# Kernel optimization log

Hardware: AMD Instinct MI355X
Metric: run time of the kernel (lower is better)

Reference implementation:

```python
import jax, jax.numpy as jnp
import numpy as np

IN_FEATS, N_HIDDEN, NUM_LAYERS, N_CLASSES, CLS_HIDDEN = 166, 76, 2, 2, 510
T, N, E = 3, 100000, 1600000
RRELU_SLOPE = (1.0 / 8.0 + 1.0 / 3.0) / 2.0  # eval-mode RReLU = leaky relu with mean slope


def setup_inputs() -> dict:
    key = jax.random.key(0)
    ks = jax.random.split(key, 24)
    d = {}
    d['feats'] = jax.random.normal(ks[0], (T, N, IN_FEATS), jnp.float32)
    d['src'] = jax.random.randint(ks[1], (T, E), 0, N, jnp.int32)
    d['dst'] = jax.random.randint(ks[2], (T, E), 0, N, jnp.int32)
    # TopK scorers (uniform +-1/sqrt(feats))
    s0 = 1.0 / np.sqrt(IN_FEATS)
    s1 = 1.0 / np.sqrt(N_HIDDEN)
    d['scorer0'] = jax.random.uniform(ks[3], (IN_FEATS, 1), jnp.float32, -s0, s0)
    d['scorer1'] = jax.random.uniform(ks[4], (N_HIDDEN, 1), jnp.float32, -s1, s1)
    # GCN weights (xavier-ish)
    d['gcn_w0'] = jax.random.normal(ks[5], (IN_FEATS, N_HIDDEN), jnp.float32) * np.sqrt(2.0 / (IN_FEATS + N_HIDDEN))
    d['gcn_w1'] = jax.random.normal(ks[6], (N_HIDDEN, N_HIDDEN), jnp.float32) * np.sqrt(2.0 / (2 * N_HIDDEN))
    # GRU params, torch layout: W_ih [3H, H_in], W_hh [3H, H], gate order (r, z, n)
    g = 1.0 / np.sqrt(N_HIDDEN)
    H3 = 3 * N_HIDDEN
    d['gru0_wih'] = jax.random.uniform(ks[7], (H3, N_HIDDEN), jnp.float32, -g, g)
    d['gru0_whh'] = jax.random.uniform(ks[8], (H3, N_HIDDEN), jnp.float32, -g, g)
    d['gru0_bih'] = jax.random.uniform(ks[9], (H3,), jnp.float32, -g, g)
    d['gru0_bhh'] = jax.random.uniform(ks[10], (H3,), jnp.float32, -g, g)
    d['gru1_wih'] = jax.random.uniform(ks[11], (H3, N_HIDDEN), jnp.float32, -g, g)
    d['gru1_whh'] = jax.random.uniform(ks[12], (H3, N_HIDDEN), jnp.float32, -g, g)
    d['gru1_bih'] = jax.random.uniform(ks[13], (H3,), jnp.float32, -g, g)
    d['gru1_bhh'] = jax.random.uniform(ks[14], (H3,), jnp.float32, -g, g)
    # MLP
    m1 = 1.0 / np.sqrt(N_HIDDEN)
    m2 = 1.0 / np.sqrt(CLS_HIDDEN)
    d['mlp_w1'] = jax.random.uniform(ks[15], (N_HIDDEN, CLS_HIDDEN), jnp.float32, -m1, m1)
    d['mlp_b1'] = jax.random.uniform(ks[16], (CLS_HIDDEN,), jnp.float32, -m1, m1)
    d['mlp_w2'] = jax.random.uniform(ks[17], (CLS_HIDDEN, N_CLASSES), jnp.float32, -m2, m2)
    d['mlp_b2'] = jax.random.uniform(ks[18], (N_CLASSES,), jnp.float32, -m2, m2)
    return d


def _topk_pool(x, scorer, k):
    # x: [N, F]; returns X_tilde: [F, k]
    scores = (x @ scorer).ravel() / jnp.linalg.norm(scorer)
    vals, idx = jax.lax.top_k(scores, k)
    out = x[idx] * jnp.tanh(vals)[:, None]  # [k, F]
    return out.T


def _gru_step(x, h, wih, whh, bih, bhh):
    # x: [B, H_in], h: [B, H]; torch GRU gate order r, z, n
    gx = x @ wih.T + bih
    gh = h @ whh.T + bhh
    H = h.shape[1]
    rx, zx, nx = gx[:, :H], gx[:, H:2 * H], gx[:, 2 * H:]
    rh, zh, nh = gh[:, :H], gh[:, H:2 * H], gh[:, 2 * H:]
    r = jax.nn.sigmoid(rx + rh)
    z = jax.nn.sigmoid(zx + zh)
    n = jnp.tanh(nx + r * nh)
    return (1.0 - z) * n + z * h


def _graph_conv(x, W, src, dst, n_nodes):
    # DGL GraphConv, norm='both', bias=False, RReLU (eval) activation
    deg_out = jnp.zeros((n_nodes,), x.dtype).at[src].add(1.0)
    deg_in = jnp.zeros((n_nodes,), x.dtype).at[dst].add(1.0)
    norm_src = jnp.clip(deg_out, 1.0, None) ** -0.5
    norm_dst = jnp.clip(deg_in, 1.0, None) ** -0.5
    h = (x * norm_src[:, None]) @ W  # project first (small out dim)
    agg = jax.ops.segment_sum(h[src], dst, num_segments=n_nodes)
    out = agg * norm_dst[:, None]
    return jnp.where(out >= 0, out, out * RRELU_SLOPE)


def reference(feats, src, dst, scorer0, scorer1, gcn_w0, gcn_w1,
              gru0_wih, gru0_whh, gru0_bih, gru0_bhh,
              gru1_wih, gru1_whh, gru1_bih, gru1_bhh,
              mlp_w1, mlp_b1, mlp_w2, mlp_b2):
    scorers = [scorer0, scorer1]
    gcn_ws = [gcn_w0, gcn_w1]
    grus = [(gru0_wih, gru0_whh, gru0_bih, gru0_bhh),
            (gru1_wih, gru1_whh, gru1_bih, gru1_bhh)]
    feat_list = [feats[t] for t in range(T)]
    for i in range(NUM_LAYERS):
        W = gcn_ws[i]
        wih, whh, bih, bhh = grus[i]
        for t in range(T):
            x_tilde = _topk_pool(feat_list[t], scorers[i], N_HIDDEN)  # [F, k]
            W = _gru_step(x_tilde, W, wih, whh, bih, bhh)  # evolve weights
            feat_list[t] = _graph_conv(feat_list[t], W, src[t], dst[t], N)
    h = feat_list[-1]
    h = jax.nn.relu(h @ mlp_w1 + mlp_b1)
    return h @ mlp_w2 + mlp_b2
```

## Files before the change

kernel.cpp:

```cpp
#include <hip/hip_runtime.h>
#include <math.h>

#define NN 100000
#define EE 1600000
#define F0 166
#define HID 76
#define H3 228
#define CHID 510
#define SLOPE 0.22916666666666666f
#define CAND_MAX 4096
#define NBIN 4096
#define HPAD 20
#define MJ 256

#define BSH 9
#define BSZ 512
#define NBKT 196
#define CH 4096
#define NCHK 391

__device__ __forceinline__ unsigned f2key(float f){
    unsigned u = __float_as_uint(f);
    return (u & 0x80000000u) ? ~u : (u | 0x80000000u);
}
__device__ __forceinline__ float key2f(unsigned k){
    unsigned u = (k & 0x80000000u) ? (k & 0x7fffffffu) : ~k;
    return __uint_as_float(u);
}

__global__ void scorer_norms_k(const float* __restrict__ s0, const float* __restrict__ s1,
                               float* __restrict__ outn){
    __shared__ float red[256];
    int tid = threadIdx.x;
    float a = 0.f;
    for (int k = tid; k < F0; k += 256) a += s0[k]*s0[k];
    red[tid] = a; __syncthreads();
    for (int s = 128; s > 0; s >>= 1){ if (tid < s) red[tid] += red[tid+s]; __syncthreads(); }
    if (tid == 0) outn[0] = 1.0f/sqrtf(red[0]);
    __syncthreads();
    float b = 0.f;
    for (int k = tid; k < HID; k += 256) b += s1[k]*s1[k];
    red[tid] = b; __syncthreads();
    for (int s = 128; s > 0; s >>= 1){ if (tid < s) red[tid] += red[tid+s]; __syncthreads(); }
    if (tid == 0) outn[1] = 1.0f/sqrtf(red[0]);
}

__global__ void pad_k(const float* __restrict__ w1, const float* __restrict__ b1,
                      const float* __restrict__ w2, float* __restrict__ w1t,
                      float* __restrict__ b1p, float* __restrict__ w2p){
    int idx = blockIdx.x*256 + threadIdx.x;
    if (idx < 512*HID){
        int j = idx / HID, k = idx - j*HID;
        w1t[idx] = (j < CHID) ? w1[k*CHID + j] : 0.f;
    }
    if (idx < 512)  b1p[idx] = (idx < CHID)   ? b1[idx] : 0.f;
    if (idx < 1024) w2p[idx] = (idx < CHID*2) ? w2[idx] : 0.f;
}


__global__ __launch_bounds__(256) void p1_hist_k(const int* __restrict__ src, const int* __restrict__ dst,
                                                 int* __restrict__ bhS, int* __restrict__ bhD){
    __shared__ int hS[NBKT], hD[NBKT];
    int t = blockIdx.y, blk = blockIdx.x, tid = threadIdx.x;
    for (int i = tid; i < NBKT; i += 256){ hS[i] = 0; hD[i] = 0; }
    __syncthreads();
    size_t ebase = (size_t)t*EE + (size_t)blk*CH;
    int m = EE - blk*CH; if (m > CH) m = CH;
    for (int j = tid; j < m; j += 256){
        atomicAdd(&hS[src[ebase + j] >> BSH], 1);
        atomicAdd(&hD[dst[ebase + j] >> BSH], 1);
    }
    __syncthreads();
    for (int i = tid; i < NBKT; i += 256){
        bhS[((size_t)t*NBKT + i)*NCHK + blk] = hS[i];
        bhD[((size_t)t*NBKT + i)*NCHK + blk] = hD[i];
    }
}

__global__ __launch_bounds__(512) void p2_scan_k(int* __restrict__ bhS, int* __restrict__ bhD,
                                                 int* __restrict__ ctS, int* __restrict__ ctD){
    __shared__ int sd[512];
    int b = blockIdx.x, t = blockIdx.y, tid = threadIdx.x;
    for (int a = 0; a < 2; a++){
        int* bh = a ? bhD : bhS;
        int* ct = a ? ctD : ctS;
        int* row = bh + ((size_t)t*NBKT + b)*NCHK;
        int v = (tid < NCHK) ? row[tid] : 0;
        sd[tid] = v; __syncthreads();
        for (int off = 1; off < 512; off <<= 1){
            int x = (tid >= off) ? sd[tid - off] : 0;
            __syncthreads();
            sd[tid] += x;
            __syncthreads();
        }
        if (tid < NCHK) row[tid] = sd[tid] - v;
        if (tid == 511) ct[t*NBKT + b] = sd[511];
        __syncthreads();
    }
}

__global__ __launch_bounds__(256) void p3_base_k(const int* __restrict__ ctS, const int* __restrict__ ctD,
                                                 int* __restrict__ bbS, int* __restrict__ bbD){
    __shared__ int sd[256];
    int tid = threadIdx.x;
    for (int a = 0; a < 2; a++){
        const int* ct = a ? ctD : ctS;
        int* bb = a ? bbD : bbS;
        for (int t = 0; t < 3; t++){
            int v = (tid < NBKT) ? ct[t*NBKT + tid] : 0;
            sd[tid] = v; __syncthreads();
            for (int off = 1; off < 256; off <<= 1){
                int x = (tid >= off) ? sd[tid - off] : 0;
                __syncthreads();
                sd[tid] += x;
                __syncthreads();
            }
            if (tid < NBKT) bb[t*(NBKT+1) + tid] = sd[tid] - v;
            if (tid == 0)   bb[t*(NBKT+1) + NBKT] = EE;
            __syncthreads();
        }
    }
}

__global__ __launch_bounds__(256) void p4_scatter_k(const int* __restrict__ src, const int* __restrict__ dst,
                                                    const int* __restrict__ bhS, const int* __restrict__ bhD,
                                                    const int* __restrict__ bbS, const int* __restrict__ bbD,
                                                    int* __restrict__ srcpart,
                                                    unsigned long long* __restrict__ pairpart){
    __shared__ int baseS[NBKT], baseD[NBKT], cS[NBKT], cD[NBKT];
    int t = blockIdx.y, blk = blockIdx.x, tid = threadIdx.x;
    for (int i = tid; i < NBKT; i += 256){
        baseS[i] = bbS[t*(NBKT+1) + i] + bhS[((size_t)t*NBKT + i)*NCHK + blk];
        baseD[i] = bbD[t*(NBKT+1) + i] + bhD[((size_t)t*NBKT + i)*NCHK + blk];
        cS[i] = 0; cD[i] = 0;
    }
    __syncthreads();
    size_t ebase = (size_t)t*EE + (size_t)blk*CH;
    int m = EE - blk*CH; if (m > CH) m = CH;
    int* sp = srcpart + (size_t)t*EE;
    unsigned long long* pp = pairpart + (size_t)t*EE;
    for (int j = tid; j < m; j += 256){
        int s = src[ebase + j], d = dst[ebase + j];
        int bs = s >> BSH, bd = d >> BSH;
        int r0 = atomicAdd(&cS[bs], 1);
        sp[baseS[bs] + r0] = s;
        int r1 = atomicAdd(&cD[bd], 1);
        pp[baseD[bd] + r1] = ((unsigned long long)(unsigned)s << 32) | (unsigned)d;
    }
}

__global__ __launch_bounds__(256) void p5_degO_k(const int* __restrict__ srcpart,
                                                 const int* __restrict__ bbS,
                                                 float* __restrict__ nO){
    __shared__ int cnt[BSZ];
    int b = blockIdx.x, t = blockIdx.y, tid = threadIdx.x;
    for (int i = tid; i < BSZ; i += 256) cnt[i] = 0;
    __syncthreads();
    int st = bbS[t*(NBKT+1) + b], en = bbS[t*(NBKT+1) + b + 1];
    const int* sp = srcpart + (size_t)t*EE;
    for (int j = st + tid; j < en; j += 256) atomicAdd(&cnt[sp[j] & (BSZ-1)], 1);
    __syncthreads();
    int nb = b << BSH;
    for (int i = tid; i < BSZ; i += 256){
        int n = nb + i;
        if (n < NN){
            int o = cnt[i]; if (o < 1) o = 1;
            nO[t*NN + n] = 1.0f/sqrtf((float)o);
        }
    }
}

__global__ __launch_bounds__(512) void p6_csr_k(const unsigned long long* __restrict__ pairpart,
                                                const int* __restrict__ bbD,
                                                int* __restrict__ degI, int* __restrict__ rs,
                                                float* __restrict__ nI,
                                                int* __restrict__ col){
    __shared__ int cnt[BSZ];
    __shared__ int sc[BSZ];
    __shared__ int fc[BSZ];
    int b = blockIdx.x, t = blockIdx.y, tid = threadIdx.x;
    cnt[tid] = 0; fc[tid] = 0;
    __syncthreads();
    int st = bbD[t*(NBKT+1) + b], en = bbD[t*(NBKT+1) + b + 1];
    const unsigned long long* pp = pairpart + (size_t)t*EE;
    for (int j = st + tid; j < en; j += 512)
        atomicAdd(&cnt[(int)(pp[j] & (unsigned long long)(BSZ-1))], 1);
    __syncthreads();
    int v = cnt[tid];
    sc[tid] = v; __syncthreads();
    for (int off = 1; off < 512; off <<= 1){
        int x = (tid >= off) ? sc[tid - off] : 0;
        __syncthreads();
        sc[tid] += x;
        __syncthreads();
    }
    int ex = sc[tid] - v;
    int nb = b << BSH;
    int n = nb + tid;
    if (n < NN){
        degI[t*NN + n] = v;
        rs[t*NN + n] = st + ex;
        int ii = v; if (ii < 1) ii = 1;
        nI[t*NN + n] = 1.0f/sqrtf((float)ii);
    }
    sc[tid] = ex;
    __syncthreads();
    int* ct = col + (size_t)t*EE;
    for (int j = st + tid; j < en; j += 512){
        unsigned long long p = pp[j];
        int d = (int)(p & 0xffffffffull);
        int li = d & (BSZ-1);
        int r = atomicAdd(&fc[li], 1);
        ct[st + sc[li] + r] = (int)(p >> 32);
    }
}


template<int F, int PAD>
__global__ __launch_bounds__(256) void score_k(const float* __restrict__ x,
                                               const float* __restrict__ scorer,
                                               const float* __restrict__ invn,
                                               float* __restrict__ scores,
                                               unsigned* hist){
    __shared__ float xs[64*PAD];
    __shared__ float part[256];
    int tid = threadIdx.x;
    int n0 = blockIdx.x*64;
    int nodes = NN - n0; if (nodes > 64) nodes = 64;
    for (int idx = tid; idx < nodes*F; idx += 256){
        int n = idx / F, k = idx - n*F;
        xs[n*PAD + k] = x[(size_t)(n0+n)*F + k];
    }
    __syncthreads();
    int w = __builtin_amdgcn_readfirstlane(tid >> 6);
    int lane = tid & 63;
    int k0 = (F*w) >> 2, k1 = (F*(w+1)) >> 2;
    const float* xrow = xs + lane*PAD;
    float s = 0.f;
    for (int k = k0; k < k1; k++) s += xrow[k]*scorer[k];
    part[w*64 + lane] = s;
    __syncthreads();
    if (tid < 64 && n0 + tid < NN){
        float tot = (part[tid] + part[64+tid] + part[128+tid] + part[192+tid]) * invn[0];
        scores[n0 + tid] = tot;
        atomicAdd(&hist[f2key(tot) >> 20], 1u);
    }
}

__global__ __launch_bounds__(256) void compact_k(const float* __restrict__ scores,
                                                 const unsigned* __restrict__ hist,
                                                 float* __restrict__ cv, int* __restrict__ ci, int* cnt){
    __shared__ unsigned cs[256];
    __shared__ int thr_s;
    int tid = threadIdx.x;
    unsigned s = 0;
    int base = NBIN - 1 - tid*16;
    for (int j = 0; j < 16; j++) s += hist[base - j];
    cs[tid] = s; __syncthreads();
    if (tid == 0){
        unsigned acc = 0; int c = 0;
        for (; c < 256; c++){ if (acc + cs[c] >= 76u) break; acc += cs[c]; }
        int b = NBIN - 1 - c*16;
        int sel = 0;
        for (int j = 0; j < 16; j++){
            acc += hist[b - j];
            if (acc >= 76u){ sel = b - j; break; }
        }
        thr_s = sel;
    }
    __syncthreads();
    int thr = thr_s;
    int n = blockIdx.x*256 + tid;
    if (n >= NN) return;
    float sv = scores[n];
    if ((int)(f2key(sv) >> 20) >= thr){
        int p = atomicAdd(cnt, 1);
        if (p < CAND_MAX){ cv[p] = sv; ci[p] = n; }
    }
}

__global__ __launch_bounds__(256) void topk_k(const float* __restrict__ cv,
                                              const int* __restrict__ ci,
                                              const int* __restrict__ cnt,
                                              int* __restrict__ topidx,
                                              float* __restrict__ tanhv){
    __shared__ unsigned long long keys[CAND_MAX];
    int tid = threadIdx.x;
    int M = *cnt; if (M > CAND_MAX) M = CAND_MAX;
    for (int i = tid; i < M; i += 256)
        keys[i] = ((unsigned long long)f2key(cv[i]) << 32) | (unsigned)(~ci[i]);
    __syncthreads();
    for (int i = tid; i < M; i += 256){
        unsigned long long ki = keys[i];
        int r = 0;
        for (int j = 0; j < M; j++) r += (keys[j] > ki) ? 1 : 0;
        if (r < 76){
            topidx[r] = (int)(~(unsigned)(ki & 0xffffffffu));
            tanhv[r]  = tanhf(key2f((unsigned)(ki >> 32)));
        }
    }
}

template<int F>
__global__ void gru_k(const float* __restrict__ cur, const int* __restrict__ topidx,
                      const float* __restrict__ tanhv, float* __restrict__ W,
                      float* __restrict__ Wt,
                      const float* __restrict__ wih, const float* __restrict__ whh,
                      const float* __restrict__ bih, const float* __restrict__ bhh){
    __shared__ float xr[HID], hr[HID], gx[H3], gh[H3];
    int r = blockIdx.x, tid = threadIdx.x;
    if (tid < HID){
        xr[tid] = cur[(size_t)topidx[tid]*F + r] * tanhv[tid];
        hr[tid] = W[r*HID + tid];
    }
    __syncthreads();
    if (tid < H3){
        const float* wi = wih + tid*HID;
        const float* wh = whh + tid*HID;
        float sa = 0.f, sb = 0.f;
        for (int k = 0; k < HID; k++){ sa += xr[k]*wi[k]; sb += hr[k]*wh[k]; }
        gx[tid] = bih[tid] + sa;
        gh[tid] = bhh[tid] + sb;
    }
    __syncthreads();
    if (tid < HID){
        float rr = 1.f/(1.f + expf(-(gx[tid] + gh[tid])));
        float zz = 1.f/(1.f + expf(-(gx[HID+tid] + gh[HID+tid])));
        float nn = tanhf(gx[2*HID+tid] + rr*gh[2*HID+tid]);
        float nv = (1.f - zz)*nn + zz*hr[tid];
        W[r*HID + tid] = nv;
        int c = tid >> 2, i = tid & 3;
        Wt[(c*F + r)*4 + i] = nv;
    }
}

template<int F, int PAD, int NB>
__global__ __launch_bounds__(256) void gemm_k(const float* __restrict__ x,
                                              const float* __restrict__ Wt,
                                              const float* __restrict__ nO,
                                              float* __restrict__ h){
    __shared__ __align__(16) float xs[NB*PAD];
    int tid = threadIdx.x;
    int n0 = blockIdx.x*NB;
    int nodes = NN - n0; if (nodes > NB) nodes = NB;
    for (int idx = tid; idx < nodes*F; idx += 256){
        int n = idx / F, k = idx - n*F;
        xs[n*PAD + k] = x[(size_t)(n0+n)*F + k];
    }
    __syncthreads();
    int w = __builtin_amdgcn_readfirstlane(tid >> 6);
    int lane = tid & 63;
    int c0 = w*5;
    const float4* Wt4 = (const float4*)Wt;
    float4 accA[5], accB[5];
    #pragma unroll
    for (int c = 0; c < 5; c++){
        accA[c] = make_float4(0.f,0.f,0.f,0.f);
        accB[c] = make_float4(0.f,0.f,0.f,0.f);
    }
    const float* xA = xs + lane*PAD;
    const float* xB = xs + ((NB==128) ? (lane+64)*PAD : lane*PAD);
    for (int k = 0; k < F; k++){
        float xa = xA[k];
        float xb = 0.f;
        if constexpr (NB == 128) xb = xB[k];
        #pragma unroll
        for (int c = 0; c < 5; c++){
            float4 wv = Wt4[(c0 + c)*F + k];
            accA[c].x += xa*wv.x; accA[c].y += xa*wv.y;
            accA[c].z += xa*wv.z; accA[c].w += xa*wv.w;
            if constexpr (NB == 128){
                accB[c].x += xb*wv.x; accB[c].y += xb*wv.y;
                accB[c].z += xb*wv.z; accB[c].w += xb*wv.w;
            }
        }
    }
    int nc = (w == 3) ? 4 : 5;
    int nA = n0 + lane;
    if (nA < NN){
        float nm = nO[nA];
        float4* h4 = (float4*)h + (size_t)nA*HPAD + c0;
        for (int c = 0; c < nc; c++){
            float4 a = accA[c];
            h4[c] = make_float4(a.x*nm, a.y*nm, a.z*nm, a.w*nm);
        }
    }
    if constexpr (NB == 128){
        int nB = n0 + 64 + lane;
        if (nB < NN){
            float nm = nO[nB];
            float4* h4 = (float4*)h + (size_t)nB*HPAD + c0;
            for (int c = 0; c < nc; c++){
                float4 a = accB[c];
                h4[c] = make_float4(a.x*nm, a.y*nm, a.z*nm, a.w*nm);
            }
        }
    }
}

__global__ void agg_k(const int* __restrict__ rs, const int* __restrict__ degI,
                      const int* __restrict__ col, const float* __restrict__ h,
                      const float* __restrict__ nI, float* __restrict__ ft){
    int idx = blockIdx.x*256 + threadIdx.x;
    if (idx >= NN*19) return;
    int n = idx/19, c = idx - n*19;
    int st = rs[n], cnt = degI[n];
    const float4* h4 = (const float4*)h;
    float ax=0.f, ay=0.f, az=0.f, aw=0.f;
    int e = 0;
    for (; e + 4 <= cnt; e += 4){
        int s0 = col[st + e];
        int s1 = col[st + e + 1];
        int s2 = col[st + e + 2];
        int s3 = col[st + e + 3];
        float4 v0 = h4[(size_t)s0*HPAD + c];
        float4 v1 = h4[(size_t)s1*HPAD + c];
        float4 v2 = h4[(size_t)s2*HPAD + c];
        float4 v3 = h4[(size_t)s3*HPAD + c];
        ax += (v0.x + v1.x) + (v2.x + v3.x);
        ay += (v0.y + v1.y) + (v2.y + v3.y);
        az += (v0.z + v1.z) + (v2.z + v3.z);
        aw += (v0.w + v1.w) + (v2.w + v3.w);
    }
    for (; e < cnt; e++){
        int s = col[st + e];
        float4 v = h4[(size_t)s*HPAD + c];
        ax += v.x; ay += v.y; az += v.z; aw += v.w;
    }
    float nm = nI[n];
    ax*=nm; ay*=nm; az*=nm; aw*=nm;
    ax = ax >= 0.f ? ax : ax*SLOPE;
    ay = ay >= 0.f ? ay : ay*SLOPE;
    az = az >= 0.f ? az : az*SLOPE;
    aw = aw >= 0.f ? aw : aw*SLOPE;
    ((float4*)ft)[(size_t)n*19 + c] = make_float4(ax,ay,az,aw);
}

__global__ __launch_bounds__(1024) void mlp2_k(const float* __restrict__ ft,
                                               const float* __restrict__ w1t,
                                               const float* __restrict__ b1p,
                                               const float* __restrict__ w2p,
                                               const float* __restrict__ b2,
                                               float* __restrict__ out){
    __shared__ __align__(16) float ws[MJ*HID];
    __shared__ float w2s[MJ*2];
    __shared__ float b1s[MJ];
    int tid = threadIdx.x;
    int jbase = blockIdx.y * MJ;
    const float4* wg = (const float4*)(w1t + (size_t)jbase*HID);
    float4* wsv = (float4*)ws;
    for (int i = tid; i < MJ*HID/4; i += 1024) wsv[i] = wg[i];
    if (tid < MJ*2) w2s[tid] = w2p[jbase*2 + tid];
    if (tid < MJ)   b1s[tid] = b1p[jbase + tid];
    __syncthreads();
    int node = blockIdx.x*1024 + tid;
    if (node >= NN) return;
    float4 r[19];
    const float4* rp = (const float4*)(ft + (size_t)node*HID);
    #pragma unroll
    for (int k = 0; k < 19; k++) r[k] = rp[k];
    float acc0 = 0.f, acc1 = 0.f;
    if (jbase == 0){ acc0 = b2[0]; acc1 = b2[1]; }
    const float4* ws4 = (const float4*)ws;
    for (int g = 0; g < MJ/4; g++){
        int j0 = g*4;
        float s0 = b1s[j0], s1 = b1s[j0+1], s2 = b1s[j0+2], s3 = b1s[j0+3];
        const float4* wr = ws4 + j0*19;
        #pragma unroll
        for (int k4 = 0; k4 < 19; k4++){
            float4 rv = r[k4];
            float4 w0 = wr[k4];
            float4 w1 = wr[19 + k4];
            float4 w2v = wr[38 + k4];
            float4 w3 = wr[57 + k4];
            s0 += rv.x*w0.x + rv.y*w0.y + rv.z*w0.z + rv.w*w0.w;
            s1 += rv.x*w1.x + rv.y*w1.y + rv.z*w1.z + rv.w*w1.w;
            s2 += rv.x*w2v.x + rv.y*w2v.y + rv.z*w2v.z + rv.w*w2v.w;
            s3 += rv.x*w3.x + rv.y*w3.y + rv.z*w3.z + rv.w*w3.w;
        }
        s0 = fmaxf(s0, 0.f); s1 = fmaxf(s1, 0.f);
        s2 = fmaxf(s2, 0.f); s3 = fmaxf(s3, 0.f);
        acc0 += s0*w2s[j0*2]   + s1*w2s[j0*2+2] + s2*w2s[j0*2+4] + s3*w2s[j0*2+6];
        acc1 += s0*w2s[j0*2+1] + s1*w2s[j0*2+3] + s2*w2s[j0*2+5] + s3*w2s[j0*2+7];
    }
    atomicAdd(&out[(size_t)node*2],     acc0);
    atomicAdd(&out[(size_t)node*2 + 1], acc1);
}

extern "C" void kernel_launch(void* const* d_in, const int* in_sizes, int n_in,
                              void* d_out, int out_size, void* d_ws, size_t ws_size,
                              hipStream_t stream)
{
    (void)in_sizes; (void)n_in; (void)out_size; (void)ws_size;
    const float* feats   = (const float*)d_in[0];
    const int*   src     = (const int*)d_in[1];
    const int*   dst     = (const int*)d_in[2];
    const float* scorer0 = (const float*)d_in[3];
    const float* scorer1 = (const float*)d_in[4];
    const float* gcnw[2] = {(const float*)d_in[5],  (const float*)d_in[6]};
    const float* wih[2]  = {(const float*)d_in[7],  (const float*)d_in[11]};
    const float* whh[2]  = {(const float*)d_in[8],  (const float*)d_in[12]};
    const float* bih[2]  = {(const float*)d_in[9],  (const float*)d_in[13]};
    const float* bhh[2]  = {(const float*)d_in[10], (const float*)d_in[14]};
    const float* w1 = (const float*)d_in[15];
    const float* b1 = (const float*)d_in[16];
    const float* w2 = (const float*)d_in[17];
    const float* b2 = (const float*)d_in[18];
    float* out = (float*)d_out;

    char* p = (char*)d_ws;
    auto alloc = [&](size_t bytes) -> void* {
        void* r = (void*)p;
        p += (bytes + 255) & ~(size_t)255;
        return r;
    };
    float* ft[3];
    for (int t = 0; t < 3; t++) ft[t] = (float*)alloc((size_t)NN*HID*4);
    float* hbuf    = (float*)alloc((size_t)NN*HPAD*16);
    int*   col_all = (int*)alloc((size_t)3*EE*4);
    float* nO_all  = (float*)alloc((size_t)3*NN*4);
    float* nI_all  = (float*)alloc((size_t)3*NN*4);
    int*   rs_all  = (int*)alloc((size_t)3*NN*4);
    int*   dI_all  = (int*)alloc((size_t)3*NN*4);
    int* srcpart = (int*)alloc((size_t)3*EE*4);
    unsigned long long* pairpart = (unsigned long long*)alloc((size_t)3*EE*8);
    int* bhS = (int*)alloc((size_t)3*NBKT*NCHK*4);
    int* bhD = (int*)alloc((size_t)3*NBKT*NCHK*4);
    int* ctS = (int*)alloc((size_t)3*NBKT*4);
    int* ctD = (int*)alloc((size_t)3*NBKT*4);
    int* bbS = (int*)alloc((size_t)3*(NBKT+1)*4);
    int* bbD = (int*)alloc((size_t)3*(NBKT+1)*4);

    float*    scores = (float*)alloc((size_t)NN*4);
    float*    cv     = (float*)alloc(CAND_MAX*4);
    int*      ci     = (int*)alloc(CAND_MAX*4);
    int*      topidx = (int*)alloc(128*4);
    float*    tanhv  = (float*)alloc(128*4);
    float*    Wbuf   = (float*)alloc((size_t)F0*HID*4 + 256);
    float*    Wt     = (float*)alloc((size_t)19*F0*16 + 4096);
    float*    invn   = (float*)alloc(256);
    float*    w1t    = (float*)alloc((size_t)512*HID*4);
    float*    b1p    = (float*)alloc(512*4);
    float*    w2p    = (float*)alloc(1024*4);

    char* zbase = p;
    unsigned* hist6 = (unsigned*)alloc((size_t)6*NBIN*4);
    int*      ccnt6 = (int*)alloc(6*256);
    size_t zsize = (size_t)(p - zbase);

    const int gN  = (NN + 255)/256;
    const int gA  = (NN*19 + 255)/256;
    const int gB  = (NN + 63)/64;
    const int gB2 = (NN + 127)/128;
    const int gM  = (NN + 1023)/1024;
    const int gP  = (512*HID + 255)/256;

    hipMemsetAsync(zbase, 0, zsize, stream);
    hipMemsetAsync(out, 0, (size_t)NN*2*4, stream);
    scorer_norms_k<<<1,256,0,stream>>>(scorer0, scorer1, invn);
    pad_k<<<gP,256,0,stream>>>(w1, b1, w2, w1t, b1p, w2p);

    p1_hist_k<<<dim3(NCHK,3),256,0,stream>>>(src, dst, bhS, bhD);
    p2_scan_k<<<dim3(NBKT,3),512,0,stream>>>(bhS, bhD, ctS, ctD);
    p3_base_k<<<1,256,0,stream>>>(ctS, ctD, bbS, bbD);
    p4_scatter_k<<<dim3(NCHK,3),256,0,stream>>>(src, dst, bhS, bhD, bbS, bbD, srcpart, pairpart);
    p5_degO_k<<<dim3(NBKT,3),256,0,stream>>>(srcpart, bbS, nO_all);
    p6_csr_k<<<dim3(NBKT,3),512,0,stream>>>(pairpart, bbD, dI_all, rs_all, nI_all, col_all);

    for (int i = 0; i < 2; i++){
        hipMemcpyAsync(Wbuf, gcnw[i], (size_t)((i==0)?F0:HID)*HID*4, hipMemcpyDeviceToDevice, stream);
        for (int t = 0; t < 3; t++){
            int q = i*3 + t;
            unsigned* hist = hist6 + (size_t)q*NBIN;
            int* ccnt = ccnt6 + q*64;
            const float* cur = (i == 0) ? (feats + (size_t)t*NN*F0) : ft[t];
            if (i == 0) score_k<F0,167><<<gB,256,0,stream>>>(cur, scorer0, invn+0, scores, hist);
            else        score_k<HID,77><<<gB,256,0,stream>>>(cur, scorer1, invn+1, scores, hist);
            compact_k<<<gN,256,0,stream>>>(scores, hist, cv, ci, ccnt);
            topk_k<<<1,256,0,stream>>>(cv, ci, ccnt, topidx, tanhv);
            if (i == 0){
                gru_k<F0><<<F0,256,0,stream>>>(cur, topidx, tanhv, Wbuf, Wt, wih[i], whh[i], bih[i], bhh[i]);
                gemm_k<F0,167,64><<<gB,256,0,stream>>>(cur, Wt, nO_all + (size_t)t*NN, hbuf);
            } else {
                gru_k<HID><<<HID,256,0,stream>>>(cur, topidx, tanhv, Wbuf, Wt, wih[i], whh[i], bih[i], bhh[i]);
                gemm_k<HID,77,128><<<gB2,256,0,stream>>>(cur, Wt, nO_all + (size_t)t*NN, hbuf);
            }
            agg_k<<<gA,256,0,stream>>>(rs_all + (size_t)t*NN, dI_all + (size_t)t*NN,
                                       col_all + (size_t)t*EE, hbuf, nI_all + (size_t)t*NN, ft[t]);
        }
    }

    mlp2_k<<<dim3(gM,2),1024,0,stream>>>(ft[2], w1t, b1p, w2p, b2, out);
}
```

Baseline: 2.587 ms.

## Register-tile the classifier MLP and band-sort CSR columns by source id

New measurement: 2.517 ms. 2.7% less time.

```diff
diff --git a/kernel.cpp b/kernel.cpp
--- a/kernel.cpp
+++ b/kernel.cpp
@@ -11,13 +11,13 @@
 #define CAND_MAX 4096
 #define NBIN 4096
 #define HPAD 20
-#define MJ 256
 
 #define BSH 9
 #define BSZ 512
 #define NBKT 196
 #define CH 4096
 #define NCHK 391
+#define NBAND 13
 
 __device__ __forceinline__ unsigned f2key(float f){
     unsigned u = __float_as_uint(f);
@@ -175,43 +175,56 @@
                                                 int* __restrict__ degI, int* __restrict__ rs,
                                                 float* __restrict__ nI,
                                                 int* __restrict__ col){
-    __shared__ int cnt[BSZ];
-    __shared__ int sc[BSZ];
-    __shared__ int fc[BSZ];
+    __shared__ int cnt2[BSZ*NBAND];
+    __shared__ int fc2[BSZ*NBAND];
+    __shared__ int sd[BSZ];
     int b = blockIdx.x, t = blockIdx.y, tid = threadIdx.x;
-    cnt[tid] = 0; fc[tid] = 0;
+    for (int i = tid; i < BSZ*NBAND; i += 512){ cnt2[i] = 0; fc2[i] = 0; }
     __syncthreads();
     int st = bbD[t*(NBKT+1) + b], en = bbD[t*(NBKT+1) + b + 1];
     const unsigned long long* pp = pairpart + (size_t)t*EE;
-    for (int j = st + tid; j < en; j += 512)
-        atomicAdd(&cnt[(int)(pp[j] & (unsigned long long)(BSZ-1))], 1);
-    __syncthreads();
-    int v = cnt[tid];
-    sc[tid] = v; __syncthreads();
+    for (int j = st + tid; j < en; j += 512){
+        unsigned long long p = pp[j];
+        int li   = (int)(p & (unsigned long long)(BSZ-1));
+        int band = (int)(p >> 32) >> 13;
+        atomicAdd(&cnt2[li*NBAND + band], 1);
+    }
+    __syncthreads();
+    int rowcnt = 0;
+    #pragma unroll
+    for (int bb = 0; bb < NBAND; bb++) rowcnt += cnt2[tid*NBAND + bb];
+    sd[tid] = rowcnt; __syncthreads();
     for (int off = 1; off < 512; off <<= 1){
-        int x = (tid >= off) ? sc[tid - off] : 0;
+        int x = (tid >= off) ? sd[tid - off] : 0;
         __syncthreads();
-        sc[tid] += x;
+        sd[tid] += x;
         __syncthreads();
     }
-    int ex = sc[tid] - v;
+    int rowEx = sd[tid] - rowcnt;
+    int run = rowEx;
+    #pragma unroll
+    for (int bb = 0; bb < NBAND; bb++){
+        int cvv = cnt2[tid*NBAND + bb];
+        cnt2[tid*NBAND + bb] = run;
+        run += cvv;
+    }
     int nb = b << BSH;
     int n = nb + tid;
     if (n < NN){
-        degI[t*NN + n] = v;
-        rs[t*NN + n] = st + ex;
-        int ii = v; if (ii < 1) ii = 1;
+        degI[t*NN + n] = rowcnt;
+        rs[t*NN + n] = st + rowEx;
+        int ii = rowcnt; if (ii < 1) ii = 1;
         nI[t*NN + n] = 1.0f/sqrtf((float)ii);
     }
-    sc[tid] = ex;
     __syncthreads();
     int* ct = col + (size_t)t*EE;
     for (int j = st + tid; j < en; j += 512){
         unsigned long long p = pp[j];
-        int d = (int)(p & 0xffffffffull);
-        int li = d & (BSZ-1);
-        int r = atomicAdd(&fc[li], 1);
-        ct[st + sc[li] + r] = (int)(p >> 32);
+        int s  = (int)(p >> 32);
+        int li = (int)(p & (unsigned long long)(BSZ-1));
+        int band = s >> 13;
+        int r = atomicAdd(&fc2[li*NBAND + band], 1);
+        ct[st + cnt2[li*NBAND + band] + r] = s;
     }
 }
 
@@ -436,55 +449,103 @@
     ((float4*)ft)[(size_t)n*19 + c] = make_float4(ax,ay,az,aw);
 }
 
-__global__ __launch_bounds__(1024) void mlp2_k(const float* __restrict__ ft,
-                                               const float* __restrict__ w1t,
-                                               const float* __restrict__ b1p,
-                                               const float* __restrict__ w2p,
-                                               const float* __restrict__ b2,
-                                               float* __restrict__ out){
-    __shared__ __align__(16) float ws[MJ*HID];
-    __shared__ float w2s[MJ*2];
-    __shared__ float b1s[MJ];
+__global__ __launch_bounds__(512) void mlp3_k(const float* __restrict__ ft,
+                                              const float* __restrict__ w1t,
+                                              const float* __restrict__ b1p,
+                                              const float* __restrict__ w2p,
+                                              const float* __restrict__ b2,
+                                              float* __restrict__ out){
+    __shared__ __align__(16) float xs[128*HID];
+    __shared__ __align__(16) float ws[256*HID];
+    __shared__ float b1s[512];
+    __shared__ float w2s[1024];
     int tid = threadIdx.x;
-    int jbase = blockIdx.y * MJ;
-    const float4* wg = (const float4*)(w1t + (size_t)jbase*HID);
-    float4* wsv = (float4*)ws;
-    for (int i = tid; i < MJ*HID/4; i += 1024) wsv[i] = wg[i];
-    if (tid < MJ*2) w2s[tid] = w2p[jbase*2 + tid];
-    if (tid < MJ)   b1s[tid] = b1p[jbase + tid];
-    __syncthreads();
-    int node = blockIdx.x*1024 + tid;
-    if (node >= NN) return;
-    float4 r[19];
-    const float4* rp = (const float4*)(ft + (size_t)node*HID);
+    int n0 = blockIdx.x*128;
+    {
+        int lim = ((NN - n0 < 128) ? (NN - n0) : 128)*19;
+        const float4* g4 = (const float4*)(ft + (size_t)n0*HID);
+        float4* s4 = (float4*)xs;
+        for (int i = tid; i < 128*19; i += 512)
+            s4[i] = (i < lim) ? g4[i] : make_float4(0.f,0.f,0.f,0.f);
+    }
+    b1s[tid] = b1p[tid];
+    for (int i = tid; i < 1024; i += 512) w2s[i] = w2p[i];
+    int wid = tid >> 6, lane = tid & 63;
+    int wr = wid >> 2, wc = wid & 3;
+    int a = lane >> 3, b = lane & 7;
+    float p0[8], p1[8];
     #pragma unroll
-    for (int k = 0; k < 19; k++) r[k] = rp[k];
-    float acc0 = 0.f, acc1 = 0.f;
-    if (jbase == 0){ acc0 = b2[0]; acc1 = b2[1]; }
-    const float4* ws4 = (const float4*)ws;
-    for (int g = 0; g < MJ/4; g++){
-        int j0 = g*4;
-        float s0 = b1s[j0], s1 = b1s[j0+1], s2 = b1s[j0+2], s3 = b1s[j0+3];
-        const float4* wr = ws4 + j0*19;
+    for (int i = 0; i < 8; i++){ p0[i] = 0.f; p1[i] = 0.f; }
+    const float4* xbase = (const float4*)(xs + (wr*64 + a)*HID);
+    for (int jb = 0; jb < 2; jb++){
+        __syncthreads();
+        {
+            const float4* g4 = (const float4*)(w1t + (size_t)jb*256*HID);
+            float4* s4 = (float4*)ws;
+            for (int i = tid; i < 256*19; i += 512) s4[i] = g4[i];
+        }
+        __syncthreads();
+        float acc[8][8];
         #pragma unroll
+        for (int i = 0; i < 8; i++)
+            #pragma unroll
+            for (int m = 0; m < 8; m++) acc[i][m] = 0.f;
+        const float4* wbase = (const float4*)(ws + (wc*64 + b)*HID);
         for (int k4 = 0; k4 < 19; k4++){
-            float4 rv = r[k4];
-            float4 w0 = wr[k4];
-            float4 w1 = wr[19 + k4];
-            float4 w2v = wr[38 + k4];
-            float4 w3 = wr[57 + k4];
-            s0 += rv.x*w0.x + rv.y*w0.y + rv.z*w0.z + rv.w*w0.w;
-            s1 += rv.x*w1.x + rv.y*w1.y + rv.z*w1.z + rv.w*w1.w;
-            s2 += rv.x*w2v.x + rv.y*w2v.y + rv.z*w2v.z + rv.w*w2v.w;
-            s3 += rv.x*w3.x + rv.y*w3.y + rv.z*w3.z + rv.w*w3.w;
-        }
-        s0 = fmaxf(s0, 0.f); s1 = fmaxf(s1, 0.f);
-        s2 = fmaxf(s2, 0.f); s3 = fmaxf(s3, 0.f);
-        acc0 += s0*w2s[j0*2]   + s1*w2s[j0*2+2] + s2*w2s[j0*2+4] + s3*w2s[j0*2+6];
-        acc1 += s0*w2s[j0*2+1] + s1*w2s[j0*2+3] + s2*w2s[j0*2+5] + s3*w2s[j0*2+7];
-    }
-    atomicAdd(&out[(size_t)node*2],     acc0);
-    atomicAdd(&out[(size_t)node*2 + 1], acc1);
+            float4 xv[8], wv[8];
+            #pragma unroll
+            for (int i = 0; i < 8; i++) xv[i] = xbase[i*(8*19) + k4];
+            #pragma unroll
+            for (int m = 0; m < 8; m++) wv[m] = wbase[m*(8*19) + k4];
+            #pragma unroll
+            for (int i = 0; i < 8; i++)
+                #pragma unroll
+                for (int m = 0; m < 8; m++){
+                    acc[i][m] += xv[i].x*wv[m].x + xv[i].y*wv[m].y
+                               + xv[i].z*wv[m].z + xv[i].w*wv[m].w;
+                }
+        }
+        #pragma unroll
+        for (int m = 0; m < 8; m++){
+            int j = jb*256 + wc*64 + b + 8*m;
+            float bias = b1s[j - jb*256 + ((jb) ? 256 : 0)];
+            bias = b1s[j];
+            float u0 = w2s[2*j], u1 = w2s[2*j+1];
+            #pragma unroll
+            for (int i = 0; i < 8; i++){
+                float s = acc[i][m] + bias;
+                s = fmaxf(s, 0.f);
+                p0[i] += s*u0;
+                p1[i] += s*u1;
+            }
+        }
+    }
+    #pragma unroll
+    for (int off = 1; off < 8; off <<= 1){
+        #pragma unroll
+        for (int i = 0; i < 8; i++){
+            p0[i] += __shfl_xor(p0[i], off, 64);
+            p1[i] += __shfl_xor(p1[i], off, 64);
+        }
+    }
+    __syncthreads();
+    float* red = xs;
+    if (b == 0){
+        #pragma unroll
+        for (int i = 0; i < 8; i++){
+            int nl = wr*64 + a + 8*i;
+            red[(wc*128 + nl)*2 + 0] = p0[i];
+            red[(wc*128 + nl)*2 + 1] = p1[i];
+        }
+    }
+    __syncthreads();
+    if (tid < 256){
+        int nl = tid >> 1, comp = tid & 1;
+        float v = red[(0*128 + nl)*2 + comp] + red[(1*128 + nl)*2 + comp]
+                + red[(2*128 + nl)*2 + comp] + red[(3*128 + nl)*2 + comp] + b2[comp];
+        int n = n0 + nl;
+        if (n < NN) out[(size_t)n*2 + comp] = v;
+    }
 }
 
 extern "C" void kernel_launch(void* const* d_in, const int* in_sizes, int n_in,
@@ -552,11 +613,10 @@
     const int gA  = (NN*19 + 255)/256;
     const int gB  = (NN + 63)/64;
     const int gB2 = (NN + 127)/128;
-    const int gM  = (NN + 1023)/1024;
+    const int gM  = (NN + 127)/128;
     const int gP  = (512*HID + 255)/256;
 
     hipMemsetAsync(zbase, 0, zsize, stream);
-    hipMemsetAsync(out, 0, (size_t)NN*2*4, stream);
     scorer_norms_k<<<1,256,0,stream>>>(scorer0, scorer1, invn);
     pad_k<<<gP,256,0,stream>>>(w1, b1, w2, w1t, b1p, w2p);
 
@@ -590,5 +650,5 @@
         }
     }
 
-    mlp2_k<<<dim3(gM,2),1024,0,stream>>>(ft[2], w1t, b1p, w2p, b2, out);
-}
+    mlp3_k<<<gM,512,0,stream>>>(ft[2], w1t, b1p, w2p, b2, out);
+}
```
